# Kernel optimization log

Measured on AMD Instinct MI355X. Metric: run time of the kernel, lower is better.

Reference implementation:

```python
import jax, jax.numpy as jnp
import numpy as np


def build_entangle(n):
    """Fixed entangling unitary: ring of CNOTs composed with H on every qubit.
    Real-valued 2^n x 2^n matrix (all gates real)."""
    D = 1 << n
    H = np.array([[1.0, 1.0], [1.0, -1.0]], np.float32) / np.float32(np.sqrt(2.0))
    Hn = np.array([[1.0]], np.float32)
    for _ in range(n):
        Hn = np.kron(Hn, H)
    # CNOT ring as a permutation of basis states (qubit 0 = most significant bit)
    idx = np.arange(D)
    pairs = [(i, i + 1) for i in range(n - 1)] + [(n - 1, 0)]
    for c, t in pairs:
        bit = (idx >> (n - 1 - c)) & 1
        idx = idx ^ (bit << (n - 1 - t))
    E = np.empty((D, D), np.float32)
    E[idx] = Hn  # P @ Hn where P|b> = |perm(b)>
    return jnp.asarray(E)


def setup_inputs() -> dict:
    key = jax.random.key(0)
    k1, k2 = jax.random.split(key)
    B, C, L = 8, 3, 2048
    K = 3
    n = C * K  # 9 qubits
    O = 8      # out_channels
    x = jax.random.normal(k1, (B, C, L), dtype=jnp.float32)
    theta = jax.random.normal(k2, (O, n), dtype=jnp.float32)  # one RY layer per output channel
    entangle = build_entangle(n)
    return {"x": x, "entangle": entangle, "theta": theta}


def _ry(t):
    c, s = jnp.cos(t / 2), jnp.sin(t / 2)
    return jnp.stack([jnp.stack([c, -s]), jnp.stack([s, c])])  # [2,2]


def reference(x, entangle, theta):
    B, C, L = x.shape
    O, n = theta.shape
    K = n // C
    D = 1 << n
    Lout = L - K + 1

    # im2col: unfold last dim, concat channels along last axis -> rows of length C*K
    win = jnp.arange(Lout)[:, None] + jnp.arange(K)[None, :]
    cols = x[:, :, win]                                   # [B, C, Lout, K]
    cols = cols.transpose(0, 2, 1, 3).reshape(B * Lout, n)  # [N, n]
    N = B * Lout

    # angle-encode each row as product state prod_i RY(x_i)|0> (real amplitudes)
    c = jnp.cos(cols / 2)
    s = jnp.sin(cols / 2)
    state = jnp.ones((N, 1), x.dtype)
    for i in range(n):  # fixed small loop over qubits
        amp = jnp.stack([c[:, i], s[:, i]], axis=-1)      # [N, 2]
        state = (state[:, :, None] * amp[:, None, :]).reshape(N, -1)
    # shared entangling layer (same for every output channel)
    state = state @ entangle.T                            # [N, D]

    def channel(th):
        st = state
        for i in range(n):  # learnable per-qubit RY layer
            g = _ry(th[i])
            st = st.reshape(N, 1 << i, 2, -1)
            st = jnp.einsum('ab,nlbr->nlar', g, st).reshape(N, D)
        st = st @ entangle.T
        p = st.reshape(N, 2, D // 2)
        return jnp.sum(p[:, 0] ** 2, -1) - jnp.sum(p[:, 1] ** 2, -1)  # <Z_0>, [N]

    out = jax.vmap(channel)(theta)                        # [O, N]
    return out.reshape(O, B, Lout).transpose(1, 0, 2)     # [B, O, Lout]
```

## Files before the change

### kernel.cpp

```cpp
#include <hip/hip_runtime.h>

#define Bq   8
#define Lx   2048
#define Oo   8
#define LOUT 2046
#define NWIN (Bq * LOUT)
#define XTOT (Bq * 3 * Lx)

#define WS_TH 0
#define WS_WC 160
#define WS_WS (160 + XTOT)

__global__ __launch_bounds__(256) void precomp(const float* __restrict__ x,
                                               const float* __restrict__ theta,
                                               float* __restrict__ ws) {
    int t = blockIdx.x * 256 + threadIdx.x;
    if (t < 128) {
        int o = t >> 4, i = t & 15;
        float v;
        if (i < 8) v = cosf(theta[o * 9 + 8 - i]);
        else       v = sinf(theta[o * 9 + 8 - (i - 8)]);
        ws[WS_TH + t] = v;
    }
    if (t < XTOT) {
        float a = 0.5f * x[t];
        float c = cosf(a), s = sinf(a);
        ws[WS_WC + t] = (c + s) * 0.70710678118654752f;
        ws[WS_WS + t] = (c - s) * 0.70710678118654752f;
    }
}

#define DPP_XOR1 0xB1
#define DPP_XOR2 0x4E
template<int CTRL>
__device__ __forceinline__ float dppf(float x) {
    int i = __float_as_int(x);
    return __int_as_float(__builtin_amdgcn_update_dpp(i, i, CTRL, 0xF, 0xF, true));
}

__global__ __launch_bounds__(256) void qconv(const float* __restrict__ ws,
                                             float* __restrict__ out) {
    const int gt   = blockIdx.x * 256 + threadIdx.x;
    const int lane = threadIdx.x & 63;
    const int a0 = lane & 1, b0 = (lane >> 1) & 1;
    const int o  = (lane >> 2) & 7;
    const int widx = gt >> 5;
    const int b = widx / LOUT;
    const int l = widx - b * LOUT;

    float w0[9], w1[9];
    const int xb = b * (3 * Lx) + l;
#pragma unroll
    for (int c = 0; c < 3; ++c)
#pragma unroll
        for (int k = 0; k < 3; ++k) {
            w0[c*3+k] = ws[WS_WC + xb + c * Lx + k];
            w1[c*3+k] = ws[WS_WS + xb + c * Lx + k];
        }
    const float* TH = ws + WS_TH + o * 16;
    float C[8], S[8];
#pragma unroll
    for (int j = 0; j < 8; ++j) { C[j] = TH[j]; S[j] = TH[8 + j]; }

    float wa0 = a0 ? w1[8] : w0[8], wa1 = a0 ? w0[8] : w1[8];
    float wb0 = b0 ? w1[8] : w0[8], wb1 = b0 ? w0[8] : w1[8];
    float B00 = (a0 ^ b0) ? C[0] : (a0 ? -S[0] : S[0]);
    float ra0 = B00 * wa0, ra1 = B00 * wa1;
    float r00 = ra0 * wb0, r01 = ra0 * wb1, r10 = ra1 * wb0, r11 = ra1 * wb1;

#pragma unroll
    for (int j = 1; j <= 6; ++j) {
        const float u0 = w0[8 - j], u1 = w1[8 - j];
        float t00 = S[j] * r00, t01 = C[j] * r01;
        float t10 = C[j] * r10, t11 = -S[j] * r11;
        float z00 = fmaf(u0, t00, u1 * t10), z10 = fmaf(u1, t00, u0 * t10);
        float z01 = fmaf(u0, t01, u1 * t11), z11 = fmaf(u1, t01, u0 * t11);
        r00 = fmaf(u0, z00, u1 * z01); r01 = fmaf(u1, z00, u0 * z01);
        r10 = fmaf(u0, z10, u1 * z11); r11 = fmaf(u1, z10, u0 * z11);
    }

    float t00 = S[7] * r00, t01 = C[7] * r01;
    float t10 = C[7] * r10, t11 = -S[7] * r11;
    float p0 = a0 ? w1[1] : w0[1], p1 = a0 ? w0[1] : w1[1];
    float q0 = b0 ? w1[1] : w0[1], q1 = b0 ? w0[1] : w1[1];
    float A0 = (a0 ? w1[0] : w0[0]) * (b0 ? w1[0] : w0[0]);
    float A1 = (a0 ? w0[0] : w1[0]) * (b0 ? w0[0] : w1[0]);
    float term1 = fmaf(p0, fmaf(q0, t00, q1 * t01), p1 * fmaf(q0, t10, q1 * t11));
    float term2 = fmaf(p1, fmaf(q1, t00, q0 * t01), p0 * fmaf(q1, t10, q0 * t11));
    float acc = fmaf(A0, term1, A1 * term2);

    acc += dppf<DPP_XOR1>(acc);
    acc += dppf<DPP_XOR2>(acc);

    if ((lane & 3) == 0)
        out[b * (Oo * LOUT) + o * LOUT + l] = acc;
}

extern "C" void kernel_launch(void* const* d_in, const int* in_sizes, int n_in,
                              void* d_out, int out_size, void* d_ws, size_t ws_size,
                              hipStream_t stream) {
    const float* x     = (const float*)d_in[0];
    const float* theta = (const float*)d_in[2];
    float* ws = (float*)d_ws;
    float* o  = (float*)d_out;

    hipLaunchKernelGGL(precomp, dim3(XTOT / 256), dim3(256), 0, stream, x, theta, ws);
    hipLaunchKernelGGL(qconv,   dim3(NWIN * 32 / 256), dim3(256), 0, stream, ws, o);
}
```

Measured before the change: 61.42 us.

## Fuse trig precompute into main kernel via shared memory staging

Removes the separate precompute kernel and its global workspace round trip. Each block now computes cos/sin encodings for its 8 windows and the theta rotations directly into shared memory, syncs once, and then runs the same per-lane contraction. This drops one kernel launch and the workspace traffic. In exchange, neighbouring windows recompute the same trig values (about 3x redundancy per x element), and every block recomputes the theta values and pays a barrier.

```diff
diff --git a/kernel.cpp b/kernel.cpp
--- a/kernel.cpp
+++ b/kernel.cpp
@@ -5,30 +5,6 @@
 #define Oo   8
 #define LOUT 2046
 #define NWIN (Bq * LOUT)
-#define XTOT (Bq * 3 * Lx)
-
-#define WS_TH 0
-#define WS_WC 160
-#define WS_WS (160 + XTOT)
-
-__global__ __launch_bounds__(256) void precomp(const float* __restrict__ x,
-                                               const float* __restrict__ theta,
-                                               float* __restrict__ ws) {
-    int t = blockIdx.x * 256 + threadIdx.x;
-    if (t < 128) {
-        int o = t >> 4, i = t & 15;
-        float v;
-        if (i < 8) v = cosf(theta[o * 9 + 8 - i]);
-        else       v = sinf(theta[o * 9 + 8 - (i - 8)]);
-        ws[WS_TH + t] = v;
-    }
-    if (t < XTOT) {
-        float a = 0.5f * x[t];
-        float c = cosf(a), s = sinf(a);
-        ws[WS_WC + t] = (c + s) * 0.70710678118654752f;
-        ws[WS_WS + t] = (c - s) * 0.70710678118654752f;
-    }
-}
 
 #define DPP_XOR1 0xB1
 #define DPP_XOR2 0x4E
@@ -38,29 +14,46 @@
     return __int_as_float(__builtin_amdgcn_update_dpp(i, i, CTRL, 0xF, 0xF, true));
 }
 
-__global__ __launch_bounds__(256) void qconv(const float* __restrict__ ws,
+__global__ __launch_bounds__(256) void qconv(const float* __restrict__ x,
+                                             const float* __restrict__ theta,
                                              float* __restrict__ out) {
-    const int gt   = blockIdx.x * 256 + threadIdx.x;
-    const int lane = threadIdx.x & 63;
+    __shared__ float sw0[8][12], sw1[8][12];
+    __shared__ float sC[8][8], sS[8][8];
+
+    const int tid  = threadIdx.x;
+    const int blk0 = blockIdx.x * 8;
+
+    if (tid < 72) {
+        int win = tid / 9, f = tid - win * 9;
+        int widx = blk0 + win;
+        int b = widx / LOUT, l = widx - b * LOUT;
+        int c = f / 3, k = f - c * 3;
+        float a = 0.5f * x[b * (3 * Lx) + c * Lx + l + k];
+        float cs = cosf(a), sn = sinf(a);
+        sw0[win][f] = (cs + sn) * 0.70710678118654752f;
+        sw1[win][f] = (cs - sn) * 0.70710678118654752f;
+    } else if (tid < 136) {
+        int idx = tid - 72;
+        int o = idx >> 3, j = idx & 7;
+        float th = theta[o * 9 + 8 - j];
+        sC[o][j] = cosf(th);
+        sS[o][j] = sinf(th);
+    }
+    __syncthreads();
+
+    const int lane = tid & 63;
     const int a0 = lane & 1, b0 = (lane >> 1) & 1;
     const int o  = (lane >> 2) & 7;
-    const int widx = gt >> 5;
+    const int win = tid >> 5;
+    const int widx = blk0 + win;
     const int b = widx / LOUT;
     const int l = widx - b * LOUT;
 
-    float w0[9], w1[9];
-    const int xb = b * (3 * Lx) + l;
+    float w0[9], w1[9], C[8], S[8];
 #pragma unroll
-    for (int c = 0; c < 3; ++c)
+    for (int f = 0; f < 9; ++f) { w0[f] = sw0[win][f]; w1[f] = sw1[win][f]; }
 #pragma unroll
-        for (int k = 0; k < 3; ++k) {
-            w0[c*3+k] = ws[WS_WC + xb + c * Lx + k];
-            w1[c*3+k] = ws[WS_WS + xb + c * Lx + k];
-        }
-    const float* TH = ws + WS_TH + o * 16;
-    float C[8], S[8];
-#pragma unroll
-    for (int j = 0; j < 8; ++j) { C[j] = TH[j]; S[j] = TH[8 + j]; }
+    for (int j = 0; j < 8; ++j) { C[j] = sC[o][j]; S[j] = sS[o][j]; }
 
     float wa0 = a0 ? w1[8] : w0[8], wa1 = a0 ? w0[8] : w1[8];
     float wb0 = b0 ? w1[8] : w0[8], wb1 = b0 ? w0[8] : w1[8];
@@ -101,9 +94,7 @@
                               hipStream_t stream) {
     const float* x     = (const float*)d_in[0];
     const float* theta = (const float*)d_in[2];
-    float* ws = (float*)d_ws;
-    float* o  = (float*)d_out;
+    float* o = (float*)d_out;
 
-    hipLaunchKernelGGL(precomp, dim3(XTOT / 256), dim3(256), 0, stream, x, theta, ws);
-    hipLaunchKernelGGL(qconv,   dim3(NWIN * 32 / 256), dim3(256), 0, stream, ws, o);
+    hipLaunchKernelGGL(qconv, dim3(NWIN / 8), dim3(256), 0, stream, x, theta, o);
 }
```

Measured after the change: 59.85 us. 1.03x faster.
